# Kernel tuning notes

Measured on AMD Instinct MI355X. Metric: run time of the kernel, lower is better.

## Reference

```python
import jax, jax.numpy as jnp
import numpy as np
from jax import lax

# norse LIFParameters defaults: tau_syn_inv=200, tau_mem_inv=100, v_leak=0,
# v_th=1, v_reset=0, dt=0.001; alpha=0.5 (super-spike surrogate slope).
DT = 1e-3
TAU_SYN_INV = 200.0
TAU_MEM_INV = 100.0
V_LEAK = 0.0
V_TH = 1.0
V_RESET = 0.0
ALPHA = 0.5
NUM_STEPS = 100


@jax.custom_vjp
def heaviside_super(x):
    # forward: hard threshold; backward: SuperSpike surrogate (norse.threshold)
    return (x > 0).astype(x.dtype)

def _hs_fwd(x):
    return heaviside_super(x), x

def _hs_bwd(x, g):
    return (g / (ALPHA * jnp.abs(x) + 1.0) ** 2,)

heaviside_super.defvjp(_hs_fwd, _hs_bwd)


def lif_step(cur, v, i):
    # norse lif_step: Euler update of membrane v and synaptic current i
    v_dec = v + DT * TAU_MEM_INV * ((V_LEAK - v) + i)
    i_dec = i * (1.0 - DT * TAU_SYN_INV)
    z = heaviside_super(v_dec - V_TH)
    v_new = (1.0 - z) * v_dec + z * V_RESET
    i_new = i_dec + cur
    return z, v_new, i_new


def conv2d(x, w, b):
    y = lax.conv_general_dilated(x, w, window_strides=(1, 1), padding='VALID',
                                 dimension_numbers=('NCHW', 'OIHW', 'NCHW'))
    return y + b[None, :, None, None]


def maxpool2(x):
    return lax.reduce_window(x, -jnp.inf, lax.max, (1, 1, 2, 2), (1, 1, 2, 2), 'VALID')


def snn_forward(x, w1, b1, w2, b2, wf, bf):
    B = x.shape[0]
    # conv1(x) is identical every timestep in the torch code; hoist it.
    cur1 = maxpool2(conv2d(x, w1, b1))  # [B,13,6,6]
    v1 = jnp.zeros_like(cur1); i1 = jnp.zeros_like(cur1)
    v2 = jnp.zeros((B, w2.shape[0], 3, 3), x.dtype); i2 = jnp.zeros_like(v2)
    v3 = jnp.zeros((B, wf.shape[0]), x.dtype); i3 = jnp.zeros_like(v3)

    def step(carry, _):
        v1, i1, v2, i2, v3, i3 = carry
        spk1, v1, i1 = lif_step(cur1, v1, i1)          # [B,13,6,6]
        cur2 = conv2d(spk1, w2, b2)                    # [B,64,3,3]
        spk2, v2, i2 = lif_step(cur2, v2, i2)
        cur3 = spk2.reshape(B, -1) @ wf.T + bf         # [B,2]
        spk3, v3, i3 = lif_step(cur3, v3, i3)
        return (v1, i1, v2, i2, v3, i3), (spk3, v3)

    _, (spk3_seq, v3_seq) = lax.scan(step, (v1, i1, v2, i2, v3, i3), None, length=NUM_STEPS)
    spk_out = spk3_seq.sum(0)   # sum of output spikes over time, [B,2]
    return spk_out, v3_seq      # v3_seq = stacked mem3_record, [T,B,2]


def setup_inputs() -> dict:
    key = jax.random.key(0)
    ks = jax.random.split(key, 7)
    B = 2048
    x = jax.random.normal(ks[0], (B, 1, 16, 16), jnp.float32)
    w1 = jax.random.normal(ks[1], (13, 1, 4, 4), jnp.float32) * 0.25
    b1 = jax.random.normal(ks[2], (13,), jnp.float32) * 0.1
    w2 = jax.random.normal(ks[3], (64, 13, 4, 4), jnp.float32) * (1.0 / np.sqrt(13 * 16))
    b2 = jax.random.normal(ks[4], (64,), jnp.float32) * 0.05
    wf = jax.random.normal(ks[5], (2, 576), jnp.float32) * (1.0 / np.sqrt(576))
    bf = jax.random.normal(ks[6], (2,), jnp.float32) * 0.05
    return {"x": x, "w1": w1, "b1": b1, "w2": w2, "b2": b2, "wf": wf, "bf": bf}


def reference(x, w1, b1, w2, b2, wf, bf):
    return snn_forward(x, w1, b1, w2, b2, wf, bf)
```

## Files before the change

kernel.cpp:

```cpp
#include <hip/hip_runtime.h>


#define NSTEPS 100
#define NCHUNK 50
#define IMSTRIDE 272
#define ZIMG (48 * IMSTRIDE)
#define Z2S 612
#define Z2T (4 * Z2S)
#define Z2PAR (2 * Z2T)

typedef __attribute__((ext_vector_type(4))) int i32x4;

__device__ __forceinline__ void conv1_row(const float* __restrict__ xs,
                                          const float* __restrict__ w1s,
                                          float b1v, int y, float* cur) {
    float cr[2][12];
    #pragma unroll
    for (int rr = 0; rr < 2; ++rr) {
        const int cy = 2 * y + rr;
        #pragma unroll
        for (int cx = 0; cx < 12; ++cx) {
            float a = 0.f;
            #pragma unroll
            for (int ky = 0; ky < 4; ++ky)
            #pragma unroll
            for (int kx = 0; kx < 4; ++kx)
                a = fmaf(xs[(cy + ky) * 16 + cx + kx], w1s[ky * 4 + kx], a);
            cr[rr][cx] = a + b1v;
        }
    }
    #pragma unroll
    for (int px = 0; px < 6; ++px)
        cur[px] = fmaxf(fmaxf(cr[0][2 * px], cr[0][2 * px + 1]),
                        fmaxf(cr[1][2 * px], cr[1][2 * px + 1]));
}

__device__ __forceinline__ void lif1_row(float* v1, float* i1, const float* cur,
                                         unsigned char* pb, int ic, int y) {
    unsigned zb[6];
    #pragma unroll
    for (int xx = 0; xx < 6; ++xx) {
        const float vd = v1[xx] + 0.1f * (i1[xx] - v1[xx]);
        i1[xx] = i1[xx] * 0.8f + cur[xx];
        const bool sp = vd > 1.0f;
        v1[xx] = sp ? 0.0f : vd;
        zb[xx] = sp ? 1u : 0u;
    }
    const unsigned q0 = zb[0] | (zb[1] << 8) | (zb[2] << 16) | (zb[3] << 24);
    const unsigned q1 = zb[1] | (zb[2] << 8) | (zb[3] << 16) | (zb[4] << 24);
    const unsigned q2 = zb[2] | (zb[3] << 8) | (zb[4] << 16) | (zb[5] << 24);
    #pragma unroll
    for (int ky = 0; ky < 4; ++ky) {
        const int py = y - ky;
        if (0 <= py && py <= 2) {
            unsigned char* b = pb - ky * (3 * IMSTRIDE) + 4 * ((ky + ic) & 3);
            *(unsigned*)(b)                = q0;
            *(unsigned*)(b + IMSTRIDE)     = q1;
            *(unsigned*)(b + 2 * IMSTRIDE) = q2;
        }
    }
}

__global__ __launch_bounds__(256, 2)
void snn_kernel(const float* __restrict__ x,
                const float* __restrict__ w1,
                const float* __restrict__ b1,
                const float* __restrict__ w2,
                const float* __restrict__ b2,
                const float* __restrict__ wf,
                const float* __restrict__ bf,
                float* __restrict__ out, int B)
{
    __shared__ __align__(16) unsigned char s_im[4 * ZIMG];
    __shared__ __align__(16) unsigned short s_z2h[2 * Z2PAR];
    __shared__ __align__(16) float s_x[4 * 256];
    __shared__ __align__(16) float s_w1[13 * 16];
    __shared__ float s_b1[13];

    const int tid  = threadIdx.x;
    const int wave = tid >> 6, lane = tid & 63;
    const int quad = lane >> 4, col = lane & 15;

    ((float4*)(s_x + wave * 256))[lane] =
        ((const float4*)(x + (size_t)(blockIdx.x * 4 + wave) * 256))[lane];
    if (tid < 208) s_w1[tid] = w1[tid];
    if (tid < 13)  s_b1[tid] = b1[tid];
    for (int i = tid; i < 4 * ZIMG / 16; i += 256)
        ((uint4*)s_im)[i] = make_uint4(0, 0, 0, 0);
    __syncthreads();

    int sA, icA, yA, sB = 0, icB = 0, yB = 0;
    { const int R = tid;       sA = R / 78; int r = R - 78 * sA; icA = r / 6; yA = r - 6 * icA; }
    if (tid < 56) { const int R = tid + 256; sB = R / 78; int r = R - 78 * sB; icB = r / 6; yB = r - 6 * icB; }

    float cur1a[6], v1a[6], i1a[6], cur1b[6], v1b[6], i1b[6];
    conv1_row(s_x + sA * 256, s_w1 + icA * 16, s_b1[icA], yA, cur1a);
    if (tid < 56) conv1_row(s_x + sB * 256, s_w1 + icB * 16, s_b1[icB], yB, cur1b);
    #pragma unroll
    for (int j = 0; j < 6; ++j) { v1a[j] = i1a[j] = 0.f; v1b[j] = i1b[j] = 0.f; }

    const int pbOffA = (9 * sA + 3 * yA) * IMSTRIDE + 16 * icA;
    const int pbOffB = (9 * sB + 3 * yB) * IMSTRIDE + 16 * icB;

    i32x4 A1[4], A2[4], A3[4];
    float Mrow;
    {
        const float* wrow = w2 + (size_t)(wave * 16 + col) * 208;
        float M = 1e-20f;
        for (int k = 0; k < 208; ++k) M = fmaxf(M, fabsf(wrow[k]));
        Mrow = M;
        const float inv = 127.0f / M;
        const float q1s = M * (1.0f / 127.0f);
        const float q2s = M * (1.0f / (127.0f * 127.0f));
        #pragma unroll
        for (int kt = 0; kt < 4; ++kt) {
            i32x4 w1v = {0, 0, 0, 0}, w2v = {0, 0, 0, 0}, w3v = {0, 0, 0, 0};
            #pragma unroll
            for (int j = 0; j < 16; ++j) {
                const int kp = kt * 64 + quad * 16 + j;
                const int W = kp >> 2, kx = kp & 3;
                const int ic = W >> 2, ky = ((W & 3) - ic) & 3;
                const float w = (ic < 13) ? wrow[ic * 16 + ky * 4 + kx] : 0.f;
                const float b1f = rintf(w * inv);
                const float r1  = fmaf(b1f, -q1s, w);
                const float b2f = rintf(r1 * inv * 127.0f);
                const float r2  = fmaf(b2f, -q2s, r1);
                const float b3f = rintf(r2 * inv * 127.0f * 127.0f);
                const int wi = j >> 2, sh = (j & 3) * 8;
                w1v[wi] |= ((int)b1f & 0xFF) << sh;
                w2v[wi] |= ((int)b2f & 0xFF) << sh;
                w3v[wi] |= ((int)b3f & 0xFF) << sh;
            }
            A1[kt] = w1v; A2[kt] = w2v; A3[kt] = w3v;
        }
    }
    float sc1[4], sc2[4], sc3[4];
    #pragma unroll
    for (int r = 0; r < 4; ++r) {
        const float Mr = __shfl(Mrow, quad * 4 + r);
        sc1[r] = Mr * (1.0f / 127.0f);
        sc2[r] = Mr * (1.0f / (127.0f * 127.0f));
        sc3[r] = Mr * (1.0f / (127.0f * 127.0f * 127.0f));
    }

    float wf0[9], wf1[9];
    #pragma unroll
    for (int q = 0; q < 9; ++q) {
        wf0[q] = wf[lane * 9 + q];
        wf1[q] = wf[576 + lane * 9 + q];
    }
    const float bfv0 = bf[0], bfv1 = bf[1];
    float b2r[4];
    #pragma unroll
    for (int r = 0; r < 4; ++r) b2r[r] = b2[wave * 16 + quad * 4 + r];

    int bpo[3];
    int zwo[3];
    bool zv[3];
    #pragma unroll
    for (int nt = 0; nt < 3; ++nt) {
        const int n = nt * 16 + col;
        bpo[nt] = n * IMSTRIDE + quad * 16;
        zv[nt] = (n < 36);
        const int slz = n / 9, pos = n - slz * 9;
        zwo[nt] = slz * Z2S + pos * 68 + wave * 16 + quad * 4;
    }

    float v2[12], i2[12];
    #pragma unroll
    for (int p = 0; p < 12; ++p) { v2[p] = 0.f; i2[p] = 0.f; }
    float v3a = 0.f, i3a = 0.f, v3b = 0.f, i3b = 0.f, sum0 = 0.f, sum1 = 0.f;

    const int sG = blockIdx.x * 4 + wave;
    float* outv = out + (size_t)2 * B;

    auto fc_step = [&](const unsigned short* zs, int tp) {
        float p0 = 0.f, p1 = 0.f;
        #pragma unroll
        for (int q = 0; q < 9; ++q) {
            const float z = __uint_as_float(((unsigned)zs[q * 68 + lane]) << 16);
            p0 = fmaf(z, wf0[q], p0);
            p1 = fmaf(z, wf1[q], p1);
        }
        #pragma unroll
        for (int off = 32; off > 0; off >>= 1) {
            p0 += __shfl_xor(p0, off);
            p1 += __shfl_xor(p1, off);
        }
        const float c3a = p0 + bfv0, c3b = p1 + bfv1;
        const float vd0 = v3a + 0.1f * (i3a - v3a);
        const float vd1 = v3b + 0.1f * (i3b - v3b);
        i3a = i3a * 0.8f + c3a;
        i3b = i3b * 0.8f + c3b;
        const bool q0 = vd0 > 1.0f, q1 = vd1 > 1.0f;
        v3a = q0 ? 0.0f : vd0;
        v3b = q1 ? 0.0f : vd1;
        sum0 += q0 ? 1.0f : 0.0f;
        sum1 += q1 ? 1.0f : 0.0f;
        if (lane == 0)
            *(float2*)(outv + (size_t)tp * 2 * B + 2 * sG) = make_float2(v3a, v3b);
    };

    auto chunk = [&](int ch, int P) {
        unsigned char* zb0 = s_im + (2 * P) * ZIMG;
        unsigned char* zb1 = s_im + (2 * P + 1) * ZIMG;
        lif1_row(v1a, i1a, cur1a, zb0 + pbOffA, icA, yA);
        if (tid < 56) lif1_row(v1b, i1b, cur1b, zb0 + pbOffB, icB, yB);
        lif1_row(v1a, i1a, cur1a, zb1 + pbOffA, icA, yA);
        if (tid < 56) lif1_row(v1b, i1b, cur1b, zb1 + pbOffB, icB, yB);
        __syncthreads();

        if (ch) {
            const unsigned short* zp = s_z2h + (P ^ 1) * Z2PAR + wave * Z2S;
            fc_step(zp, 2 * ch - 2);
            fc_step(zp + Z2T, 2 * ch - 1);
        }

        #pragma unroll
        for (int tl = 0; tl < 2; ++tl) {
            const unsigned char* zbuf = s_im + (2 * P + tl) * ZIMG;
            i32x4 c1a = {0,0,0,0}, c1b = c1a, c1c = c1a;
            i32x4 c2a = c1a, c2b = c1a, c2c = c1a;
            i32x4 c3a_ = c1a, c3b_ = c1a, c3c = c1a;
            #pragma unroll
            for (int kt = 0; kt < 4; ++kt) {
                const i32x4 B0 = *(const i32x4*)(zbuf + bpo[0] + kt * 64);
                const i32x4 B1 = *(const i32x4*)(zbuf + bpo[1] + kt * 64);
                const i32x4 B2v = *(const i32x4*)(zbuf + bpo[2] + kt * 64);
                c1a = __builtin_amdgcn_mfma_i32_16x16x64_i8(A1[kt], B0,  c1a, 0, 0, 0);
                c1b = __builtin_amdgcn_mfma_i32_16x16x64_i8(A1[kt], B1,  c1b, 0, 0, 0);
                c1c = __builtin_amdgcn_mfma_i32_16x16x64_i8(A1[kt], B2v, c1c, 0, 0, 0);
                c2a = __builtin_amdgcn_mfma_i32_16x16x64_i8(A2[kt], B0,  c2a, 0, 0, 0);
                c2b = __builtin_amdgcn_mfma_i32_16x16x64_i8(A2[kt], B1,  c2b, 0, 0, 0);
                c2c = __builtin_amdgcn_mfma_i32_16x16x64_i8(A2[kt], B2v, c2c, 0, 0, 0);
                c3a_ = __builtin_amdgcn_mfma_i32_16x16x64_i8(A3[kt], B0,  c3a_, 0, 0, 0);
                c3b_ = __builtin_amdgcn_mfma_i32_16x16x64_i8(A3[kt], B1,  c3b_, 0, 0, 0);
                c3c = __builtin_amdgcn_mfma_i32_16x16x64_i8(A3[kt], B2v, c3c, 0, 0, 0);
            }

            const i32x4 L1[3] = {c1a, c1b, c1c};
            const i32x4 L2[3] = {c2a, c2b, c2c};
            const i32x4 L3[3] = {c3a_, c3b_, c3c};
            unsigned short* z2b = s_z2h + P * Z2PAR + tl * Z2T;
            #pragma unroll
            for (int nt = 0; nt < 3; ++nt) {
                unsigned zbits[4];
                #pragma unroll
                for (int r = 0; r < 4; ++r) {
                    const int p = nt * 4 + r;
                    const float cur2 =
                        fmaf(sc1[r], (float)L1[nt][r],
                        fmaf(sc2[r], (float)L2[nt][r],
                        fmaf(sc3[r], (float)L3[nt][r], b2r[r])));
                    const float vd = v2[p] + 0.1f * (i2[p] - v2[p]);
                    i2[p] = i2[p] * 0.8f + cur2;
                    const bool sp = vd > 1.0f;
                    v2[p] = sp ? 0.0f : vd;
                    zbits[r] = sp ? 0x3F80u : 0u;
                }
                if (zv[nt]) {
                    const unsigned lo = zbits[0] | (zbits[1] << 16);
                    const unsigned hi = zbits[2] | (zbits[3] << 16);
                    *(uint2*)(z2b + zwo[nt]) = make_uint2(lo, hi);
                }
            }
        }
    };

    #pragma unroll 1
    for (int cc = 0; cc < NCHUNK; cc += 2) {
        chunk(cc, 0);
        chunk(cc + 1, 1);
    }

    __syncthreads();
    {
        const unsigned short* zp = s_z2h + 1 * Z2PAR + wave * Z2S;
        fc_step(zp, NSTEPS - 2);
        fc_step(zp + Z2T, NSTEPS - 1);
    }

    if (lane == 0)
        *(float2*)(out + (size_t)2 * sG) = make_float2(sum0, sum1);
}

extern "C" void kernel_launch(void* const* d_in, const int* in_sizes, int n_in,
                              void* d_out, int out_size, void* d_ws, size_t ws_size,
                              hipStream_t stream)
{
    const float* x  = (const float*)d_in[0];
    const float* w1 = (const float*)d_in[1];
    const float* b1 = (const float*)d_in[2];
    const float* w2 = (const float*)d_in[3];
    const float* b2 = (const float*)d_in[4];
    const float* wf = (const float*)d_in[5];
    const float* bf = (const float*)d_in[6];
    float* out = (float*)d_out;

    const int B = in_sizes[0] / 256;
    const int grid = B / 4;

    hipLaunchKernelGGL(snn_kernel, dim3(grid), dim3(256), 0, stream,
                       x, w1, b1, w2, b2, wf, bf, out, B);
}
```

Baseline: 267.9 us.

## Halve samples per block, shrink LDS and registers, raise occupancy to four blocks

```diff
diff --git a/kernel.cpp b/kernel.cpp
--- a/kernel.cpp
+++ b/kernel.cpp
@@ -4,10 +4,9 @@
 #define NSTEPS 100
 #define NCHUNK 50
 #define IMSTRIDE 272
-#define ZIMG (48 * IMSTRIDE)
-#define Z2S 612
-#define Z2T (4 * Z2S)
-#define Z2PAR (2 * Z2T)
+#define NROW 18
+#define ZIMG (NROW * IMSTRIDE)
+#define Z2SLOT 1224
 
 typedef __attribute__((ext_vector_type(4))) int i32x4;
 
@@ -61,7 +60,7 @@
     }
 }
 
-__global__ __launch_bounds__(256, 2)
+__global__ __launch_bounds__(256, 4)
 void snn_kernel(const float* __restrict__ x,
                 const float* __restrict__ w1,
                 const float* __restrict__ b1,
@@ -72,35 +71,35 @@
                 float* __restrict__ out, int B)
 {
     __shared__ __align__(16) unsigned char s_im[4 * ZIMG];
-    __shared__ __align__(16) unsigned short s_z2h[2 * Z2PAR];
-    __shared__ __align__(16) float s_x[4 * 256];
-    __shared__ __align__(16) float s_w1[13 * 16];
-    __shared__ float s_b1[13];
+    __shared__ __align__(16) unsigned char s_ovl[4 * Z2SLOT];
+
+    float* const s_xf = (float*)s_ovl;
+    float* const s_w1 = (float*)(s_ovl + 2048);
+    float* const s_b1 = (float*)(s_ovl + 2880);
+    unsigned char* const s_z2 = s_ovl;
 
     const int tid  = threadIdx.x;
     const int wave = tid >> 6, lane = tid & 63;
     const int quad = lane >> 4, col = lane & 15;
 
-    ((float4*)(s_x + wave * 256))[lane] =
-        ((const float4*)(x + (size_t)(blockIdx.x * 4 + wave) * 256))[lane];
+    if (wave < 2)
+        ((float4*)(s_xf + wave * 256))[lane] =
+            ((const float4*)(x + (size_t)(blockIdx.x * 2 + wave) * 256))[lane];
     if (tid < 208) s_w1[tid] = w1[tid];
     if (tid < 13)  s_b1[tid] = b1[tid];
     for (int i = tid; i < 4 * ZIMG / 16; i += 256)
         ((uint4*)s_im)[i] = make_uint4(0, 0, 0, 0);
     __syncthreads();
 
-    int sA, icA, yA, sB = 0, icB = 0, yB = 0;
-    { const int R = tid;       sA = R / 78; int r = R - 78 * sA; icA = r / 6; yA = r - 6 * icA; }
-    if (tid < 56) { const int R = tid + 256; sB = R / 78; int r = R - 78 * sB; icB = r / 6; yB = r - 6 * icB; }
-
-    float cur1a[6], v1a[6], i1a[6], cur1b[6], v1b[6], i1b[6];
-    conv1_row(s_x + sA * 256, s_w1 + icA * 16, s_b1[icA], yA, cur1a);
-    if (tid < 56) conv1_row(s_x + sB * 256, s_w1 + icB * 16, s_b1[icB], yB, cur1b);
-    #pragma unroll
-    for (int j = 0; j < 6; ++j) { v1a[j] = i1a[j] = 0.f; v1b[j] = i1b[j] = 0.f; }
-
+    const bool rowv = tid < 156;
+    int sA = 0, icA = 0, yA = 0;
+    if (rowv) { sA = tid / 78; int r = tid - 78 * sA; icA = r / 6; yA = r - 6 * icA; }
+
+    float cur1a[6], v1a[6], i1a[6];
+    if (rowv) conv1_row(s_xf + sA * 256, s_w1 + icA * 16, s_b1[icA], yA, cur1a);
+    #pragma unroll
+    for (int j = 0; j < 6; ++j) { v1a[j] = 0.f; i1a[j] = 0.f; }
     const int pbOffA = (9 * sA + 3 * yA) * IMSTRIDE + 16 * icA;
-    const int pbOffB = (9 * sB + 3 * yB) * IMSTRIDE + 16 * icB;
 
     i32x4 A1[4], A2[4], A3[4];
     float Mrow;
@@ -154,31 +153,32 @@
     #pragma unroll
     for (int r = 0; r < 4; ++r) b2r[r] = b2[wave * 16 + quad * 4 + r];
 
-    int bpo[3];
-    int zwo[3];
-    bool zv[3];
-    #pragma unroll
-    for (int nt = 0; nt < 3; ++nt) {
+    int bpo[2];
+    int zwo[2];
+    bool zv[2];
+    #pragma unroll
+    for (int nt = 0; nt < 2; ++nt) {
         const int n = nt * 16 + col;
-        bpo[nt] = n * IMSTRIDE + quad * 16;
-        zv[nt] = (n < 36);
-        const int slz = n / 9, pos = n - slz * 9;
-        zwo[nt] = slz * Z2S + pos * 68 + wave * 16 + quad * 4;
-    }
-
-    float v2[12], i2[12];
-    #pragma unroll
-    for (int p = 0; p < 12; ++p) { v2[p] = 0.f; i2[p] = 0.f; }
+        const int nc = (n < 18) ? n : (n - 14);
+        bpo[nt] = nc * IMSTRIDE + quad * 16;
+        zv[nt] = (n < 18);
+        const int slz = nc / 9, pos = nc - 9 * slz;
+        zwo[nt] = slz * 612 + pos * 68 + wave * 16 + quad * 4;
+    }
+
+    float v2[8], i2[8];
+    #pragma unroll
+    for (int p = 0; p < 8; ++p) { v2[p] = 0.f; i2[p] = 0.f; }
     float v3a = 0.f, i3a = 0.f, v3b = 0.f, i3b = 0.f, sum0 = 0.f, sum1 = 0.f;
 
-    const int sG = blockIdx.x * 4 + wave;
+    const int sGf = blockIdx.x * 2 + (wave - 2);
     float* outv = out + (size_t)2 * B;
 
-    auto fc_step = [&](const unsigned short* zs, int tp) {
+    auto fc_step = [&](const unsigned char* zs, int tp) {
         float p0 = 0.f, p1 = 0.f;
         #pragma unroll
         for (int q = 0; q < 9; ++q) {
-            const float z = __uint_as_float(((unsigned)zs[q * 68 + lane]) << 16);
+            const float z = (float)zs[q * 68 + lane];
             p0 = fmaf(z, wf0[q], p0);
             p1 = fmaf(z, wf1[q], p1);
         }
@@ -198,53 +198,50 @@
         sum0 += q0 ? 1.0f : 0.0f;
         sum1 += q1 ? 1.0f : 0.0f;
         if (lane == 0)
-            *(float2*)(outv + (size_t)tp * 2 * B + 2 * sG) = make_float2(v3a, v3b);
+            *(float2*)(outv + (size_t)tp * 2 * B + 2 * sGf) = make_float2(v3a, v3b);
     };
 
     auto chunk = [&](int ch, int P) {
         unsigned char* zb0 = s_im + (2 * P) * ZIMG;
         unsigned char* zb1 = s_im + (2 * P + 1) * ZIMG;
-        lif1_row(v1a, i1a, cur1a, zb0 + pbOffA, icA, yA);
-        if (tid < 56) lif1_row(v1b, i1b, cur1b, zb0 + pbOffB, icB, yB);
-        lif1_row(v1a, i1a, cur1a, zb1 + pbOffA, icA, yA);
-        if (tid < 56) lif1_row(v1b, i1b, cur1b, zb1 + pbOffB, icB, yB);
+        if (rowv) {
+            lif1_row(v1a, i1a, cur1a, zb0 + pbOffA, icA, yA);
+            lif1_row(v1a, i1a, cur1a, zb1 + pbOffA, icA, yA);
+        }
         __syncthreads();
 
-        if (ch) {
-            const unsigned short* zp = s_z2h + (P ^ 1) * Z2PAR + wave * Z2S;
+        if (ch && wave >= 2) {
+            const unsigned char* zp =
+                s_z2 + ((P ^ 1) * 2) * Z2SLOT + (wave - 2) * 612;
             fc_step(zp, 2 * ch - 2);
-            fc_step(zp + Z2T, 2 * ch - 1);
+            fc_step(zp + Z2SLOT, 2 * ch - 1);
         }
 
         #pragma unroll
         for (int tl = 0; tl < 2; ++tl) {
             const unsigned char* zbuf = s_im + (2 * P + tl) * ZIMG;
-            i32x4 c1a = {0,0,0,0}, c1b = c1a, c1c = c1a;
-            i32x4 c2a = c1a, c2b = c1a, c2c = c1a;
-            i32x4 c3a_ = c1a, c3b_ = c1a, c3c = c1a;
+            i32x4 c1a = {0,0,0,0}, c1b = c1a;
+            i32x4 c2a = c1a, c2b = c1a;
+            i32x4 c3a_ = c1a, c3b_ = c1a;
             #pragma unroll
             for (int kt = 0; kt < 4; ++kt) {
                 const i32x4 B0 = *(const i32x4*)(zbuf + bpo[0] + kt * 64);
                 const i32x4 B1 = *(const i32x4*)(zbuf + bpo[1] + kt * 64);
-                const i32x4 B2v = *(const i32x4*)(zbuf + bpo[2] + kt * 64);
-                c1a = __builtin_amdgcn_mfma_i32_16x16x64_i8(A1[kt], B0,  c1a, 0, 0, 0);
-                c1b = __builtin_amdgcn_mfma_i32_16x16x64_i8(A1[kt], B1,  c1b, 0, 0, 0);
-                c1c = __builtin_amdgcn_mfma_i32_16x16x64_i8(A1[kt], B2v, c1c, 0, 0, 0);
-                c2a = __builtin_amdgcn_mfma_i32_16x16x64_i8(A2[kt], B0,  c2a, 0, 0, 0);
-                c2b = __builtin_amdgcn_mfma_i32_16x16x64_i8(A2[kt], B1,  c2b, 0, 0, 0);
-                c2c = __builtin_amdgcn_mfma_i32_16x16x64_i8(A2[kt], B2v, c2c, 0, 0, 0);
-                c3a_ = __builtin_amdgcn_mfma_i32_16x16x64_i8(A3[kt], B0,  c3a_, 0, 0, 0);
-                c3b_ = __builtin_amdgcn_mfma_i32_16x16x64_i8(A3[kt], B1,  c3b_, 0, 0, 0);
-                c3c = __builtin_amdgcn_mfma_i32_16x16x64_i8(A3[kt], B2v, c3c, 0, 0, 0);
+                c1a = __builtin_amdgcn_mfma_i32_16x16x64_i8(A1[kt], B0, c1a, 0, 0, 0);
+                c1b = __builtin_amdgcn_mfma_i32_16x16x64_i8(A1[kt], B1, c1b, 0, 0, 0);
+                c2a = __builtin_amdgcn_mfma_i32_16x16x64_i8(A2[kt], B0, c2a, 0, 0, 0);
+                c2b = __builtin_amdgcn_mfma_i32_16x16x64_i8(A2[kt], B1, c2b, 0, 0, 0);
+                c3a_ = __builtin_amdgcn_mfma_i32_16x16x64_i8(A3[kt], B0, c3a_, 0, 0, 0);
+                c3b_ = __builtin_amdgcn_mfma_i32_16x16x64_i8(A3[kt], B1, c3b_, 0, 0, 0);
             }
 
-            const i32x4 L1[3] = {c1a, c1b, c1c};
-            const i32x4 L2[3] = {c2a, c2b, c2c};
-            const i32x4 L3[3] = {c3a_, c3b_, c3c};
-            unsigned short* z2b = s_z2h + P * Z2PAR + tl * Z2T;
-            #pragma unroll
-            for (int nt = 0; nt < 3; ++nt) {
-                unsigned zbits[4];
+            const i32x4 L1[2] = {c1a, c1b};
+            const i32x4 L2[2] = {c2a, c2b};
+            const i32x4 L3[2] = {c3a_, c3b_};
+            unsigned char* z2b = s_z2 + (2 * P + tl) * Z2SLOT;
+            #pragma unroll
+            for (int nt = 0; nt < 2; ++nt) {
+                unsigned zby[4];
                 #pragma unroll
                 for (int r = 0; r < 4; ++r) {
                     const int p = nt * 4 + r;
@@ -256,13 +253,11 @@
                     i2[p] = i2[p] * 0.8f + cur2;
                     const bool sp = vd > 1.0f;
                     v2[p] = sp ? 0.0f : vd;
-                    zbits[r] = sp ? 0x3F80u : 0u;
+                    zby[r] = sp ? 1u : 0u;
                 }
-                if (zv[nt]) {
-                    const unsigned lo = zbits[0] | (zbits[1] << 16);
-                    const unsigned hi = zbits[2] | (zbits[3] << 16);
-                    *(uint2*)(z2b + zwo[nt]) = make_uint2(lo, hi);
-                }
+                if (zv[nt])
+                    *(unsigned*)(z2b + zwo[nt]) =
+                        zby[0] | (zby[1] << 8) | (zby[2] << 16) | (zby[3] << 24);
             }
         }
     };
@@ -274,14 +269,13 @@
     }
 
     __syncthreads();
-    {
-        const unsigned short* zp = s_z2h + 1 * Z2PAR + wave * Z2S;
+    if (wave >= 2) {
+        const unsigned char* zp = s_z2 + 2 * Z2SLOT + (wave - 2) * 612;
         fc_step(zp, NSTEPS - 2);
-        fc_step(zp + Z2T, NSTEPS - 1);
-    }
-
-    if (lane == 0)
-        *(float2*)(out + (size_t)2 * sG) = make_float2(sum0, sum1);
+        fc_step(zp + Z2SLOT, NSTEPS - 1);
+        if (lane == 0)
+            *(float2*)(out + (size_t)2 * sGf) = make_float2(sum0, sum1);
+    }
 }
 
 extern "C" void kernel_launch(void* const* d_in, const int* in_sizes, int n_in,
@@ -298,7 +292,7 @@
     float* out = (float*)d_out;
 
     const int B = in_sizes[0] / 256;
-    const int grid = B / 4;
+    const int grid = B / 2;
 
     hipLaunchKernelGGL(snn_kernel, dim3(grid), dim3(256), 0, stream,
                        x, w1, b1, w2, b2, wf, bf, out, B);
```

Measured after the change: 924.8 us. +245.2%, slower.
